# Kernel optimization log

Measured on AMD Instinct MI355X. Metric: run time of the kernel, lower is better.

The kernel has to match this reference:

```python
import jax, jax.numpy as jnp
import numpy as np
from jax import lax

PAD = (2, 1)  # (pad_before, pad_after) applied to both H and W


def setup_inputs() -> dict:
    key = jax.random.key(0)
    x = jax.random.normal(key, (32, 256, 64, 64), dtype=jnp.float32)
    # make_kernel([1,3,3,1]) * upsample_factor**2
    k1 = jnp.array([1.0, 3.0, 3.0, 1.0], dtype=jnp.float32)
    k2 = k1[None, :] * k1[:, None]
    k2 = k2 / jnp.sum(k2)
    k2 = k2 * 4.0  # upsample_factor ** 2 with upsample_factor = 2
    return {"x": x, "kernel": k2}


def reference(x, kernel):
    # upfirdn2d(x, kernel, up=1, down=1, pad=PAD) == pad + depthwise FIR conv.
    # FIR filtering is true convolution, so flip the kernel before using
    # lax's cross-correlation primitive (kernel is symmetric here anyway).
    n, c, h, w = x.shape
    kh, kw = kernel.shape
    xp = jnp.pad(x, ((0, 0), (0, 0), (PAD[0], PAD[1]), (PAD[0], PAD[1])))
    kf = jnp.flip(kernel, axis=(0, 1))
    # depthwise: OIHW kernel with O=C, I=1, feature_group_count=C
    wk = jnp.tile(kf[None, None, :, :], (c, 1, 1, 1))
    out = lax.conv_general_dilated(
        xp, wk,
        window_strides=(1, 1),
        padding='VALID',
        dimension_numbers=('NCHW', 'OIHW', 'NCHW'),
        feature_group_count=c,
    )
    return out  # [N, C, H + pad0 + pad1 - kh + 1, W + pad0 + pad1 - kw + 1]
```

## Files before the change

kernel.cpp:

```cpp
#include <hip/hip_runtime.h>


#define SM_STRIDE 68
#define SM_ROWS   67

__global__ __launch_bounds__(256) void Blur_910533066888_kernel(
    const float* __restrict__ x,
    const float* __restrict__ k,
    float* __restrict__ out)
{
    __shared__ float sm[SM_ROWS * SM_STRIDE];

    const int t = threadIdx.x;
    const int plane = blockIdx.x;
    const float* __restrict__ xin = x + (size_t)plane * 4096;
    float* __restrict__ op = out + (size_t)plane * 4096;

    #pragma unroll
    for (int i = 0; i < 18; ++i) {
        int idx = t + i * 256;
        if (idx < SM_ROWS * SM_STRIDE) sm[idx] = 0.0f;
    }
    __syncthreads();

    #pragma unroll
    for (int it = 0; it < 4; ++it) {
        int f4  = t + it * 256;
        int row = f4 >> 4;
        int col = (f4 & 15) << 2;
        float4 v = reinterpret_cast<const float4*>(xin)[f4];
        float* dst = &sm[(row + 2) * SM_STRIDE + (col + 2)];
        dst[0] = v.x; dst[1] = v.y; dst[2] = v.z; dst[3] = v.w;
    }

    float kf[4][4];
    #pragma unroll
    for (int i = 0; i < 4; ++i)
        #pragma unroll
        for (int j = 0; j < 4; ++j)
            kf[i][j] = k[(3 - i) * 4 + (3 - j)];

    __syncthreads();

    const int ty = (t >> 4) << 2;
    const int tx = (t & 15) << 2;

    float win[7][7];
    #pragma unroll
    for (int r = 0; r < 7; ++r)
        #pragma unroll
        for (int c = 0; c < 7; ++c)
            win[r][c] = sm[(ty + r) * SM_STRIDE + (tx + c)];

    #pragma unroll
    for (int r = 0; r < 4; ++r) {
        float a0 = 0.f, a1 = 0.f, a2 = 0.f, a3 = 0.f;
        #pragma unroll
        for (int i = 0; i < 4; ++i) {
            #pragma unroll
            for (int j = 0; j < 4; ++j) {
                const float w = kf[i][j];
                a0 = fmaf(w, win[r + i][0 + j], a0);
                a1 = fmaf(w, win[r + i][1 + j], a1);
                a2 = fmaf(w, win[r + i][2 + j], a2);
                a3 = fmaf(w, win[r + i][3 + j], a3);
            }
        }
        float4 acc = make_float4(a0, a1, a2, a3);
        *reinterpret_cast<float4*>(&op[(ty + r) * 64 + tx]) = acc;
    }
}

extern "C" void kernel_launch(void* const* d_in, const int* in_sizes, int n_in,
                              void* d_out, int out_size, void* d_ws, size_t ws_size,
                              hipStream_t stream)
{
    const float* x = (const float*)d_in[0];
    const float* k = (const float*)d_in[1];
    float* out = (float*)d_out;

    const int planes = 32 * 256;
    Blur_910533066888_kernel<<<planes, 256, 0, stream>>>(x, k, out);
}
```

Before: 44.84 us.

## Zero only halo, vectorize LDS access, stream rows into 4x4 accumulators

Drops the full shared-memory clear and its extra barrier, zeroing only the halo border cells in parallel with the interior load. Interior stores to LDS become float2 writes and window reads become float4 row reads. The 7x7 register window is replaced by row-wise streaming into 16 accumulators, and the kernel weights are read from global/constant memory inside the loop. Launch bounds add a min-blocks-per-SM hint of 8 to lower register pressure and raise occupancy, at the risk of spilling.

```diff
diff --git a/kernel.cpp b/kernel.cpp
--- a/kernel.cpp
+++ b/kernel.cpp
@@ -4,7 +4,7 @@
 #define SM_STRIDE 68
 #define SM_ROWS   67
 
-__global__ __launch_bounds__(256) void Blur_910533066888_kernel(
+__global__ __launch_bounds__(256, 8) void Blur_910533066888_kernel(
     const float* __restrict__ x,
     const float* __restrict__ k,
     float* __restrict__ out)
@@ -17,57 +17,68 @@
     float* __restrict__ op = out + (size_t)plane * 4096;
 
     #pragma unroll
-    for (int i = 0; i < 18; ++i) {
-        int idx = t + i * 256;
-        if (idx < SM_ROWS * SM_STRIDE) sm[idx] = 0.0f;
-    }
-    __syncthreads();
-
-    #pragma unroll
     for (int it = 0; it < 4; ++it) {
         int f4  = t + it * 256;
         int row = f4 >> 4;
         int col = (f4 & 15) << 2;
         float4 v = reinterpret_cast<const float4*>(xin)[f4];
-        float* dst = &sm[(row + 2) * SM_STRIDE + (col + 2)];
-        dst[0] = v.x; dst[1] = v.y; dst[2] = v.z; dst[3] = v.w;
+        float2* d = reinterpret_cast<float2*>(&sm[(row + 2) * SM_STRIDE + (col + 2)]);
+        d[0] = make_float2(v.x, v.y);
+        d[1] = make_float2(v.z, v.w);
     }
 
-    float kf[4][4];
-    #pragma unroll
-    for (int i = 0; i < 4; ++i)
-        #pragma unroll
-        for (int j = 0; j < 4; ++j)
-            kf[i][j] = k[(3 - i) * 4 + (3 - j)];
+    {
+        const float4 z4 = make_float4(0.f, 0.f, 0.f, 0.f);
+        const float2 z2 = make_float2(0.f, 0.f);
+        if (t < 34) {
+            reinterpret_cast<float4*>(sm)[t] = z4;
+        } else if (t < 51) {
+            reinterpret_cast<float4*>(sm)[1122 + (t - 34)] = z4;
+        } else if (t >= 64 && t < 128) {
+            int r = t - 62;
+            *reinterpret_cast<float2*>(&sm[r * SM_STRIDE]) = z2;
+        } else if (t >= 128 && t < 192) {
+            int r = t - 126;
+            *reinterpret_cast<float2*>(&sm[r * SM_STRIDE + 66]) = z2;
+        }
+    }
 
     __syncthreads();
 
     const int ty = (t >> 4) << 2;
     const int tx = (t & 15) << 2;
 
-    float win[7][7];
+    float acc[4][4];
     #pragma unroll
-    for (int r = 0; r < 7; ++r)
+    for (int a = 0; a < 4; ++a)
         #pragma unroll
-        for (int c = 0; c < 7; ++c)
-            win[r][c] = sm[(ty + r) * SM_STRIDE + (tx + c)];
+        for (int b = 0; b < 4; ++b)
+            acc[a][b] = 0.f;
 
     #pragma unroll
-    for (int r = 0; r < 4; ++r) {
-        float a0 = 0.f, a1 = 0.f, a2 = 0.f, a3 = 0.f;
+    for (int r = 0; r < 7; ++r) {
+        const float* srow = &sm[(ty + r) * SM_STRIDE + tx];
+        float4 w0 = *reinterpret_cast<const float4*>(srow);
+        float4 w1 = *reinterpret_cast<const float4*>(srow + 4);
+        float wr[8] = {w0.x, w0.y, w0.z, w0.w, w1.x, w1.y, w1.z, w1.w};
         #pragma unroll
-        for (int i = 0; i < 4; ++i) {
+        for (int orow = 0; orow < 4; ++orow) {
+            const int i = r - orow;
+            if (i < 0 || i > 3) continue;
             #pragma unroll
             for (int j = 0; j < 4; ++j) {
-                const float w = kf[i][j];
-                a0 = fmaf(w, win[r + i][0 + j], a0);
-                a1 = fmaf(w, win[r + i][1 + j], a1);
-                a2 = fmaf(w, win[r + i][2 + j], a2);
-                a3 = fmaf(w, win[r + i][3 + j], a3);
+                const float w = k[(3 - i) * 4 + (3 - j)];
+                #pragma unroll
+                for (int c = 0; c < 4; ++c)
+                    acc[orow][c] = fmaf(w, wr[j + c], acc[orow][c]);
             }
         }
-        float4 acc = make_float4(a0, a1, a2, a3);
-        *reinterpret_cast<float4*>(&op[(ty + r) * 64 + tx]) = acc;
+    }
+
+    #pragma unroll
+    for (int orow = 0; orow < 4; ++orow) {
+        float4 o = make_float4(acc[orow][0], acc[orow][1], acc[orow][2], acc[orow][3]);
+        *reinterpret_cast<float4*>(&op[(ty + orow) * 64 + tx]) = o;
     }
 }
 
```

After: 62.06 us. +38.4%, slower.

## Split 4x4 blur into separable horizontal and vertical passes

Applied to the files above, without the earlier changes.

The 4x4 FIR is factored into a horizontal 4-tap pass, done in registers on global loads and stored to shared memory, followed by a vertical 4-tap pass read back as float4 rows. The horizontal pass handles the left and right padding by zero-filling edge loads, so only three pad rows need clearing instead of the whole shared buffer, and one barrier is dropped. Together with fewer FMAs and vectorized LDS reads, this targets instruction and LDS overhead. The factorization assumes the kernel is rank-1 (separable) and that k[15] is nonzero, which holds for this input but not for an arbitrary 4x4 kernel.

```diff
diff --git a/kernel.cpp b/kernel.cpp
--- a/kernel.cpp
+++ b/kernel.cpp
@@ -1,73 +1,83 @@
 #include <hip/hip_runtime.h>
 
 
-#define SM_STRIDE 68
-#define SM_ROWS   67
+#define ST 68
 
-__global__ __launch_bounds__(256) void Blur_910533066888_kernel(
+__global__ __launch_bounds__(256, 8) void Blur_910533066888_kernel(
     const float* __restrict__ x,
     const float* __restrict__ k,
     float* __restrict__ out)
 {
-    __shared__ float sm[SM_ROWS * SM_STRIDE];
+    __shared__ float sm[67 * ST];
 
     const int t = threadIdx.x;
     const int plane = blockIdx.x;
     const float* __restrict__ xin = x + (size_t)plane * 4096;
     float* __restrict__ op = out + (size_t)plane * 4096;
 
-    #pragma unroll
-    for (int i = 0; i < 18; ++i) {
-        int idx = t + i * 256;
-        if (idx < SM_ROWS * SM_STRIDE) sm[idx] = 0.0f;
-    }
-    __syncthreads();
+    const float inv = 1.0f / k[15];
+    const float kw0 = k[15] * inv, kw1 = k[14] * inv, kw2 = k[13] * inv, kw3 = k[12] * inv;
+    const float kh0 = k[15], kh1 = k[11], kh2 = k[7], kh3 = k[3];
 
-    #pragma unroll
-    for (int it = 0; it < 4; ++it) {
-        int f4  = t + it * 256;
-        int row = f4 >> 4;
-        int col = (f4 & 15) << 2;
-        float4 v = reinterpret_cast<const float4*>(xin)[f4];
-        float* dst = &sm[(row + 2) * SM_STRIDE + (col + 2)];
-        dst[0] = v.x; dst[1] = v.y; dst[2] = v.z; dst[3] = v.w;
+    const int rx = t >> 2;
+    const int q  = t & 3;
+    const int cq = q << 4;
+    const float* xrow = xin + rx * 64 + cq;
+
+    float4 v0 = make_float4(0.f, 0.f, 0.f, 0.f);
+    float4 v5 = make_float4(0.f, 0.f, 0.f, 0.f);
+    if (q > 0) v0 = *reinterpret_cast<const float4*>(xrow - 4);
+    float4 v1 = *reinterpret_cast<const float4*>(xrow);
+    float4 v2 = *reinterpret_cast<const float4*>(xrow + 4);
+    float4 v3 = *reinterpret_cast<const float4*>(xrow + 8);
+    float4 v4 = *reinterpret_cast<const float4*>(xrow + 12);
+    if (q < 3) v5 = *reinterpret_cast<const float4*>(xrow + 16);
+
+    if (t < 48) {
+        int zr = t >> 4;
+        zr = (zr == 2) ? 66 : zr;
+        *reinterpret_cast<float4*>(&sm[zr * ST + ((t & 15) << 2)]) =
+            make_float4(0.f, 0.f, 0.f, 0.f);
     }
 
-    float kf[4][4];
+    float xv[24] = {
+        v0.x, v0.y, v0.z, v0.w,  v1.x, v1.y, v1.z, v1.w,
+        v2.x, v2.y, v2.z, v2.w,  v3.x, v3.y, v3.z, v3.w,
+        v4.x, v4.y, v4.z, v4.w,  v5.x, v5.y, v5.z, v5.w };
+
+    float* yd = &sm[(rx + 2) * ST + cq];
     #pragma unroll
-    for (int i = 0; i < 4; ++i)
+    for (int g = 0; g < 4; ++g) {
+        float4 yq;
+        float* yp = &yq.x;
         #pragma unroll
-        for (int j = 0; j < 4; ++j)
-            kf[i][j] = k[(3 - i) * 4 + (3 - j)];
+        for (int e = 0; e < 4; ++e) {
+            const int u = g * 4 + e;
+            yp[e] = fmaf(kw0, xv[u + 2],
+                    fmaf(kw1, xv[u + 3],
+                    fmaf(kw2, xv[u + 4], kw3 * xv[u + 5])));
+        }
+        *reinterpret_cast<float4*>(yd + 4 * g) = yq;
+    }
 
     __syncthreads();
 
     const int ty = (t >> 4) << 2;
     const int tx = (t & 15) << 2;
 
-    float win[7][7];
+    float4 w[7];
     #pragma unroll
-    for (int r = 0; r < 7; ++r)
-        #pragma unroll
-        for (int c = 0; c < 7; ++c)
-            win[r][c] = sm[(ty + r) * SM_STRIDE + (tx + c)];
+    for (int s = 0; s < 7; ++s)
+        w[s] = *reinterpret_cast<const float4*>(&sm[(ty + s) * ST + tx]);
 
     #pragma unroll
     for (int r = 0; r < 4; ++r) {
-        float a0 = 0.f, a1 = 0.f, a2 = 0.f, a3 = 0.f;
-        #pragma unroll
-        for (int i = 0; i < 4; ++i) {
-            #pragma unroll
-            for (int j = 0; j < 4; ++j) {
-                const float w = kf[i][j];
-                a0 = fmaf(w, win[r + i][0 + j], a0);
-                a1 = fmaf(w, win[r + i][1 + j], a1);
-                a2 = fmaf(w, win[r + i][2 + j], a2);
-                a3 = fmaf(w, win[r + i][3 + j], a3);
-            }
-        }
-        float4 acc = make_float4(a0, a1, a2, a3);
-        *reinterpret_cast<float4*>(&op[(ty + r) * 64 + tx]) = acc;
+        float4 o;
+        o.x = fmaf(kh0, w[r].x, fmaf(kh1, w[r+1].x, fmaf(kh2, w[r+2].x, kh3 * w[r+3].x)));
+        o.y = fmaf(kh0, w[r].y, fmaf(kh1, w[r+1].y, fmaf(kh2, w[r+2].y, kh3 * w[r+3].y)));
+        o.z = fmaf(kh0, w[r].z, fmaf(kh1, w[r+1].z, fmaf(kh2, w[r+2].z, kh3 * w[r+3].z)));
+        o.w = fmaf(kh0, w[r].w, fmaf(kh1, w[r+1].w, fmaf(kh2, w[r+2].w, kh3 * w[r+3].w)));
+        *reinterpret_cast<float4*>(&op[(ty + r) * 64 + tx]) = o;
     }
 }
 
```

Result: no change. 44.00 us (-1.9%).
